# Kernel optimization log

Hardware: AMD Instinct MI355X
Metric: run time of the kernel (lower is better)

The kernel has to match this reference:

```python
import jax, jax.numpy as jnp
import numpy as np

N = 50000
E = 800000
T = 16
F_NODE = 8
VOCAB = 30000
D_TXT = 64
H = 64
C = 2


def _gru_last(emb, w_ih, w_hh, b_ih, b_hh):
    # emb: [N, T, D_TXT] -> last hidden state [N, H] (PyTorch GRU equations)
    def step(h, xt):
        gi = xt @ w_ih.T + b_ih          # [N, 3H]
        gh = h @ w_hh.T + b_hh           # [N, 3H]
        i_r, i_z, i_n = jnp.split(gi, 3, axis=-1)
        h_r, h_z, h_n = jnp.split(gh, 3, axis=-1)
        r = jax.nn.sigmoid(i_r + h_r)
        z = jax.nn.sigmoid(i_z + h_z)
        n = jnp.tanh(i_n + r * h_n)
        h_new = (1.0 - z) * n + z * h
        return h_new, None
    h0 = jnp.zeros((emb.shape[0], H), dtype=emb.dtype)
    hT, _ = jax.lax.scan(step, h0, jnp.swapaxes(emb, 0, 1))
    return hT


def _gcn_norm(edge_index, n_nodes):
    # add self-loops, symmetric normalization (PyG GCNConv default)
    loops = jnp.arange(n_nodes, dtype=edge_index.dtype)
    row = jnp.concatenate([edge_index[0], loops])
    col = jnp.concatenate([edge_index[1], loops])
    deg = jax.ops.segment_sum(jnp.ones_like(col, dtype=jnp.float32), col,
                              num_segments=n_nodes)
    dinv = jax.lax.rsqrt(jnp.maximum(deg, 1.0))
    norm = dinv[row] * dinv[col]
    return row, col, norm


def _gcn_conv(x, row, col, norm, W, b, n_nodes):
    m = x @ W                                    # [N, H]
    msg = norm[:, None] * m[row]                 # gather + scale
    out = jax.ops.segment_sum(msg, col, num_segments=n_nodes)
    return out + b


def setup_inputs() -> dict:
    key = jax.random.key(0)
    ks = jax.random.split(key, 16)
    s = 0.05
    return {
        "x": jax.random.normal(ks[0], (N, F_NODE), dtype=jnp.float32),
        "edge_index": jax.random.randint(ks[1], (2, E), 0, N, dtype=jnp.int32),
        "xtext": jax.random.randint(ks[2], (N, T), 0, VOCAB, dtype=jnp.int32),
        "embed": jax.random.normal(ks[3], (VOCAB, D_TXT), dtype=jnp.float32),
        "w_ih": jax.random.normal(ks[4], (3 * H, D_TXT), dtype=jnp.float32) * s,
        "w_hh": jax.random.normal(ks[5], (3 * H, H), dtype=jnp.float32) * s,
        "b_ih": jnp.zeros((3 * H,), dtype=jnp.float32),
        "b_hh": jnp.zeros((3 * H,), dtype=jnp.float32),
        "W1": jax.random.normal(ks[6], (F_NODE + H, H), dtype=jnp.float32) * s,
        "b1": jnp.zeros((H,), dtype=jnp.float32),
        "W2": jax.random.normal(ks[7], (H, H), dtype=jnp.float32) * s,
        "b2": jnp.zeros((H,), dtype=jnp.float32),
        "Wl1": jax.random.normal(ks[8], (2 * H, H), dtype=jnp.float32) * s,
        "bl1": jnp.zeros((H,), dtype=jnp.float32),
        "Wf": jax.random.normal(ks[9], (H, C), dtype=jnp.float32) * s,
        "bf": jnp.zeros((C,), dtype=jnp.float32),
    }


def reference(x, edge_index, xtext, embed, w_ih, w_hh, b_ih, b_hh,
              W1, b1, W2, b2, Wl1, bl1, Wf, bf):
    n_nodes = x.shape[0]
    # text encode: embedding lookup + GRU, take last timestep
    emb = embed[xtext]                               # [N, T, D_TXT]
    textout = _gru_last(emb, w_ih, w_hh, b_ih, b_hh)  # [N, H]
    h = jnp.concatenate([x, textout], axis=1)        # [N, F_NODE+H]
    # two GCN layers with shared normalized edge structure
    row, col, norm = _gcn_norm(edge_index, n_nodes)
    h = jax.nn.relu(_gcn_conv(h, row, col, norm, W1, b1, n_nodes))
    h = jax.nn.relu(_gcn_conv(h, row, col, norm, W2, b2, n_nodes))
    # edge-pair classifier (original edges, no self-loops)
    xpair = jnp.concatenate([h[edge_index[0]], h[edge_index[1]]], axis=1)
    xpair = jax.nn.relu(xpair @ Wl1 + bl1)
    logits = xpair @ Wf + bf
    return jax.nn.log_softmax(logits, axis=1)
```

## Files before the change

kernel.cpp:

```cpp
#include <hip/hip_runtime.h>
#include <math.h>

#define N_NODES 50000
#define N_EDGES 800000
#define SCAN_NB ((N_NODES + 255) / 256)
#define VOCAB   30000
#define NT32    ((N_NODES + 31) / 32)

typedef __attribute__((ext_vector_type(8)))  short bf16x8;
typedef __attribute__((ext_vector_type(4)))  float f32x4;
typedef __attribute__((ext_vector_type(16))) float f32x16;

__device__ inline short f2bf(float f) {
    union { float f; unsigned u; } v; v.f = f;
    unsigned r = v.u + 0x7FFFu + ((v.u >> 16) & 1u);
    return (short)(r >> 16);
}
__device__ inline float bflo(unsigned u) { union { unsigned u; float f; } v; v.u = u << 16; return v.f; }
__device__ inline float bfhi(unsigned u) { union { unsigned u; float f; } v; v.u = u & 0xffff0000u; return v.f; }
__device__ inline unsigned cvtpk(float a, float b) {
    unsigned r; asm("v_cvt_pk_bf16_f32 %0, %1, %2" : "=v"(r) : "v"(a), "v"(b)); return r;
}
__device__ inline float exp2neg(float x) { float r; asm("v_exp_f32 %0, -%1" : "=v"(r) : "v"(x)); return r; }
__device__ inline float exp2p(float x)   { float r; asm("v_exp_f32 %0, %1"  : "=v"(r) : "v"(x)); return r; }

__device__ inline f32x4 mfma16(bf16x8 a, bf16x8 b, f32x4 c) {
    return __builtin_amdgcn_mfma_f32_16x16x32_bf16(a, b, c, 0, 0, 0);
}
__device__ inline f32x16 mfma32(bf16x8 a, bf16x8 b, f32x16 c) {
    return __builtin_amdgcn_mfma_f32_32x32x16_bf16(a, b, c, 0, 0, 0);
}
__device__ inline f32x16 splat16(float v) {
    f32x16 r;
    #pragma unroll
    for (int i = 0; i < 16; ++i) r[i] = v;
    return r;
}

__global__ void k_embcvt(const float* __restrict__ e, short* __restrict__ o) {
    int i = blockIdx.x * 256 + threadIdx.x;
    if (i >= VOCAB * 64 / 8) return;
    const float4* p = (const float4*)(e + i * 8);
    float4 a = p[0], b = p[1];
    bf16x8 v;
    v[0]=f2bf(a.x); v[1]=f2bf(a.y); v[2]=f2bf(a.z); v[3]=f2bf(a.w);
    v[4]=f2bf(b.x); v[5]=f2bf(b.y); v[6]=f2bf(b.z); v[7]=f2bf(b.w);
    *(bf16x8*)(o + i * 8) = v;
}

__global__ void k_count(const int* __restrict__ ei, int* __restrict__ cnt) {
    int e = blockIdx.x * 256 + threadIdx.x;
    if (e < N_EDGES) atomicAdd(&cnt[ei[N_EDGES + e]], 1);
}
__global__ void k_scan_local(const int* __restrict__ cnt, int* __restrict__ excl,
                             int* __restrict__ bsum) {
    __shared__ int s[256];
    int tid = threadIdx.x;
    int i = blockIdx.x * 256 + tid;
    int v = (i < N_NODES) ? cnt[i] : 0;
    s[tid] = v;
    __syncthreads();
    #pragma unroll
    for (int off = 1; off < 256; off <<= 1) {
        int t = (tid >= off) ? s[tid - off] : 0;
        __syncthreads();
        s[tid] += t;
        __syncthreads();
    }
    if (i < N_NODES) excl[i] = s[tid] - v;
    if (tid == 255) bsum[blockIdx.x] = s[255];
}
__global__ void k_scan_bsum(int* __restrict__ bsum) {
    __shared__ int s[256];
    int tid = threadIdx.x;
    int v = (tid < SCAN_NB) ? bsum[tid] : 0;
    s[tid] = v;
    __syncthreads();
    #pragma unroll
    for (int off = 1; off < 256; off <<= 1) {
        int t = (tid >= off) ? s[tid - off] : 0;
        __syncthreads();
        s[tid] += t;
        __syncthreads();
    }
    if (tid < SCAN_NB) bsum[tid] = s[tid] - v;
}
__global__ void k_make_starts(const int* __restrict__ excl, const int* __restrict__ bsum,
                              const int* __restrict__ cnt,
                              int* __restrict__ starts, int* __restrict__ cursor,
                              float* __restrict__ dinv) {
    int i = blockIdx.x * 256 + threadIdx.x;
    if (i >= N_NODES) return;
    int st = excl[i] + bsum[blockIdx.x];
    starts[i] = st;
    cursor[i] = st;
    dinv[i] = rsqrtf((float)cnt[i] + 1.0f);
}
__global__ void k_fill(const int* __restrict__ ei, int* __restrict__ cursor,
                       int* __restrict__ csr_src) {
    int e = blockIdx.x * 256 + threadIdx.x;
    if (e >= N_EDGES) return;
    int c = ei[N_EDGES + e];
    int p = atomicAdd(&cursor[c], 1);
    csr_src[p] = ei[e];
}

__global__ __launch_bounds__(256) void k_gru8(
    const int*   __restrict__ xtext,
    const short* __restrict__ embbf,
    const float* __restrict__ w_ih, const float* __restrict__ w_hh,
    const float* __restrict__ b_ih, const float* __restrict__ b_hh,
    unsigned* __restrict__ ht32)
{
    __shared__ short bfrag[2 * 4 * 6 * 64 * 8];
    __shared__ short hbuf[4][32 * 64];

    const int tid = threadIdx.x;
    const float L2E = 1.4426950408889634f;
    for (int u = tid; u < 3072; u += 256) {
        int l   = u & 63;
        int ct  = (u >> 6) % 6;
        int ks  = (u / 384) % 4;
        int mat = u / 1536;
        const float* W = mat ? w_hh : w_ih;
        float sc = (ct < 4) ? L2E : 2.0f * L2E;
        const float* src = &W[(ct * 32 + (l & 31)) * 64 + ks * 16 + ((l >> 5) << 3)];
        short* dst = &bfrag[u * 8];
        #pragma unroll
        for (int i = 0; i < 8; ++i) dst[i] = f2bf(src[i] * sc);
    }
    __syncthreads();

    const int lane = tid & 63;
    const int wave = tid >> 6;
    const int l5 = lane >> 5;
    const int cl = lane & 31;

    const int tile  = blockIdx.x * 4 + wave;
    if (tile >= NT32) return;
    const int nbase = tile * 32;

    float b_r[2], b_z[2], b_ni[2], b_nh[2];
    #pragma unroll
    for (int p = 0; p < 2; ++p) {
        int j = p * 32 + cl;
        b_r[p]  = (b_ih[j]        + b_hh[j])        * L2E;
        b_z[p]  = (b_ih[64 + j]   + b_hh[64 + j])   * L2E;
        b_ni[p] = b_ih[128 + j] * (2.0f * L2E);
        b_nh[p] = b_hh[128 + j] * (2.0f * L2E);
    }

    const bf16x8* BF = (const bf16x8*)bfrag;
    short* hl = &hbuf[wave][0];

    float hr0[16], hr1[16];
    #pragma unroll
    for (int g = 0; g < 16; ++g) { hr0[g] = 0.0f; hr1[g] = 0.0f; }

    const int node = min(nbase + cl, N_NODES - 1);
    const int* toks = &xtext[node * 16];

    bf16x8 eA[4], eB[4];

#define LOADE(DST, T) { int tok_ = toks[T]; const short* er_ = &embbf[tok_ * 64 + 8 * l5]; \
    DST[0] = *(const bf16x8*)(er_);      DST[1] = *(const bf16x8*)(er_ + 16); \
    DST[2] = *(const bf16x8*)(er_ + 32); DST[3] = *(const bf16x8*)(er_ + 48); }

#define STEP(T, EC, EP, FIRST, LAST) { \
    bf16x8 hA[4]; \
    if (!(FIRST)) { \
        _Pragma("unroll") \
        for (int ks = 0; ks < 4; ++ks) { \
            int o = (ks * 2 + l5) ^ (cl & 7); \
            hA[ks] = *(const bf16x8*)&hl[cl * 64 + o * 8]; \
        } \
    } \
    if (!(LAST)) LOADE(EP, (T) + 1); \
    _Pragma("unroll") \
    for (int p = 0; p < 2; ++p) { \
        f32x16 ar = splat16(b_r[p]); \
        f32x16 az = splat16(b_z[p]); \
        f32x16 ai = splat16(b_ni[p]); \
        f32x16 ah = splat16(b_nh[p]); \
        _Pragma("unroll") \
        for (int ks = 0; ks < 4; ++ks) { \
            ar = mfma32(EC[ks], BF[(ks * 6 + p) * 64 + lane], ar); \
            az = mfma32(EC[ks], BF[(ks * 6 + 2 + p) * 64 + lane], az); \
            ai = mfma32(EC[ks], BF[(ks * 6 + 4 + p) * 64 + lane], ai); \
        } \
        if (!(FIRST)) { \
            _Pragma("unroll") \
            for (int ks = 0; ks < 4; ++ks) { \
                ar = mfma32(hA[ks], BF[((4 + ks) * 6 + p) * 64 + lane], ar); \
                az = mfma32(hA[ks], BF[((4 + ks) * 6 + 2 + p) * 64 + lane], az); \
                ah = mfma32(hA[ks], BF[((4 + ks) * 6 + 4 + p) * 64 + lane], ah); \
            } \
        } \
        float* hrp = p ? hr1 : hr0; \
        _Pragma("unroll") \
        for (int g = 0; g < 16; ++g) { \
            float r = __builtin_amdgcn_rcpf(1.0f + exp2neg(ar[g])); \
            float z = __builtin_amdgcn_rcpf(1.0f + exp2neg(az[g])); \
            float v = ai[g] + r * ah[g]; \
            float n = 1.0f - 2.0f * __builtin_amdgcn_rcpf(exp2p(v) + 1.0f); \
            hrp[g] = n + z * (hrp[g] - n); \
        } \
    } \
    _Pragma("unroll") \
    for (int g = 0; g < 16; ++g) { \
        unsigned u = cvtpk(hr0[g], hr1[g]); \
        int m = (g & 3) + 8 * (g >> 2) + 4 * l5; \
        if (!(LAST)) { \
            int o0 = (cl >> 3) ^ (m & 7); \
            int o1 = (4 + (cl >> 3)) ^ (m & 7); \
            hl[m * 64 + o0 * 8 + (cl & 7)] = (short)u; \
            hl[m * 64 + o1 * 8 + (cl & 7)] = (short)(u >> 16); \
        } else { \
            int n_ = nbase + m; \
            if (n_ < N_NODES) ht32[(unsigned)n_ * 32 + cl] = u; \
        } \
    } \
}

    LOADE(eA, 0);
    STEP(0, eA, eB, true, false)

    #pragma unroll 1
    for (int tt = 0; tt < 7; ++tt) {
        int t1 = 1 + 2 * tt;
        STEP(t1,     eB, eA, false, false)
        STEP(t1 + 1, eA, eB, false, false)
    }
    STEP(15, eB, eA, false, true)

#undef STEP
#undef LOADE
}

__global__ void k_mm1(const float* __restrict__ x, const unsigned* __restrict__ ht32,
                      const float* __restrict__ W, const float* __restrict__ dinv,
                      float* __restrict__ M) {
    __shared__ float Wl[72 * 64];
    int tid = threadIdx.x;
    for (int i = tid; i < 72 * 64; i += 256) Wl[i] = W[i];
    __syncthreads();
    int j = tid & 63;
    int n = blockIdx.x * 4 + (tid >> 6);
    if (n >= N_NODES) return;
    float acc = 0.0f;
    const float* xr = x + n * 8;
    #pragma unroll
    for (int k = 0; k < 8; ++k) acc += xr[k] * Wl[k * 64 + j];
    const unsigned* hr = ht32 + (unsigned)n * 32;
    #pragma unroll
    for (int w = 0; w < 32; ++w) {
        unsigned u = hr[w];
        acc += bflo(u) * Wl[(8 + w) * 64 + j];
        acc += bfhi(u) * Wl[(8 + 32 + w) * 64 + j];
    }
    M[n * 64 + j] = dinv[n] * acc;
}

__global__ void k_mm64(const float* __restrict__ X, const float* __restrict__ W,
                       const float* __restrict__ dinv, float* __restrict__ M) {
    __shared__ float Wl[64 * 64];
    int tid = threadIdx.x;
    for (int i = tid; i < 64 * 64; i += 256) Wl[i] = W[i];
    __syncthreads();
    int j = tid & 63;
    int n = blockIdx.x * 4 + (tid >> 6);
    if (n >= N_NODES) return;
    const float* xr = X + n * 64;
    float acc = 0.0f;
    #pragma unroll
    for (int k = 0; k < 64; ++k) acc += xr[k] * Wl[k * 64 + j];
    M[n * 64 + j] = dinv[n] * acc;
}

__global__ __launch_bounds__(256) void k_gather(
    const float* __restrict__ ms, const int* __restrict__ csr_src,
    const int* __restrict__ starts, const int* __restrict__ cnt,
    const float* __restrict__ dinv, const float* __restrict__ b,
    float* __restrict__ out)
{
    int n = blockIdx.x * 4 + (threadIdx.x >> 6);
    if (n >= N_NODES) return;
    int j = threadIdx.x & 63;
    int c = cnt[n];
    const int* lst = csr_src + starts[n];
    float acc = ms[n * 64 + j];
    int k = 0;
    for (; k + 8 <= c; k += 8) {
        int r[8];
        #pragma unroll
        for (int u = 0; u < 8; ++u) r[u] = lst[k + u];
        #pragma unroll
        for (int u = 0; u < 8; ++u) acc += ms[r[u] * 64 + j];
    }
    for (; k < c; ++k) acc += ms[lst[k] * 64 + j];
    float v = dinv[n] * acc + b[j];
    out[n * 64 + j] = fmaxf(v, 0.0f);
}

__global__ __launch_bounds__(256) void k_gather_bf(
    const float* __restrict__ ms, const int* __restrict__ csr_src,
    const int* __restrict__ starts, const int* __restrict__ cnt,
    const float* __restrict__ dinv, const float* __restrict__ b,
    short* __restrict__ out)
{
    int n = blockIdx.x * 4 + (threadIdx.x >> 6);
    if (n >= N_NODES) return;
    int j = threadIdx.x & 63;
    int c = cnt[n];
    const int* lst = csr_src + starts[n];
    float acc = ms[n * 64 + j];
    int k = 0;
    for (; k + 8 <= c; k += 8) {
        int r[8];
        #pragma unroll
        for (int u = 0; u < 8; ++u) r[u] = lst[k + u];
        #pragma unroll
        for (int u = 0; u < 8; ++u) acc += ms[r[u] * 64 + j];
    }
    for (; k < c; ++k) acc += ms[lst[k] * 64 + j];
    float v = dinv[n] * acc + b[j];
    out[n * 64 + j] = f2bf(fmaxf(v, 0.0f));
}

__global__ __launch_bounds__(256) void k_edge_mfma(
    const int* __restrict__ ei, const short* __restrict__ h2b,
    const float* __restrict__ Wl1, const float* __restrict__ bl1,
    const float* __restrict__ Wf,  const float* __restrict__ bf,
    float* __restrict__ out)
{
    __shared__ float wl_s[128 * 64];
    const int tid = threadIdx.x;
    for (int i = tid; i < 128 * 64; i += 256) wl_s[i] = Wl1[i];
    __syncthreads();

    const int lane = tid & 63;
    const int wave = tid >> 6;
    const int lg = lane >> 4;
    const int ll = lane & 15;

    bf16x8 B[16];
    #pragma unroll
    for (int ks = 0; ks < 4; ++ks) {
        #pragma unroll
        for (int ct = 0; ct < 4; ++ct) {
            int c  = ct * 16 + ll;
            int kb = ks * 32 + 8 * lg;
            bf16x8 v;
            #pragma unroll
            for (int i = 0; i < 8; ++i) v[i] = f2bf(wl_s[(kb + i) * 64 + c]);
            B[ks * 4 + ct] = v;
        }
    }
    float wf0[4], wf1[4], bl[4];
    #pragma unroll
    for (int ct = 0; ct < 4; ++ct) {
        int c = ct * 16 + ll;
        wf0[ct] = Wf[c * 2 + 0];
        wf1[ct] = Wf[c * 2 + 1];
        bl[ct]  = bl1[c];
    }
    const float bf0 = bf[0], bf1 = bf[1];

    for (int tile = blockIdx.x * 4 + wave; tile < N_EDGES / 16; tile += gridDim.x * 4) {
        const int ebase = tile * 16;
        const int erow  = ebase + ll;
        const int src = ei[erow];
        const int dst = ei[N_EDGES + erow];

        f32x4 acc[4];
        #pragma unroll
        for (int ct = 0; ct < 4; ++ct) acc[ct] = (f32x4){bl[ct], bl[ct], bl[ct], bl[ct]};

        #pragma unroll
        for (int ks = 0; ks < 4; ++ks) {
            const int nd = (ks < 2) ? src : dst;
            bf16x8 A = *(const bf16x8*)&h2b[nd * 64 + (ks & 1) * 32 + 8 * lg];
            #pragma unroll
            for (int ct = 0; ct < 4; ++ct) acc[ct] = mfma16(A, B[ks * 4 + ct], acc[ct]);
        }

        float p0[4], p1[4];
        #pragma unroll
        for (int q = 0; q < 4; ++q) { p0[q] = 0.0f; p1[q] = 0.0f; }
        #pragma unroll
        for (int ct = 0; ct < 4; ++ct) {
            #pragma unroll
            for (int q = 0; q < 4; ++q) {
                float hd = fmaxf(acc[ct][q], 0.0f);
                p0[q] += hd * wf0[ct];
                p1[q] += hd * wf1[ct];
            }
        }
        #pragma unroll
        for (int m = 1; m <= 8; m <<= 1) {
            #pragma unroll
            for (int q = 0; q < 4; ++q) {
                p0[q] += __shfl_xor(p0[q], m, 64);
                p1[q] += __shfl_xor(p1[q], m, 64);
            }
        }
        if (ll < 8) {
            int q = ll >> 1, cls = ll & 1;
            float l0 = p0[q] + bf0, l1 = p1[q] + bf1;
            float mx  = fmaxf(l0, l1);
            float lse = mx + __logf(__expf(l0 - mx) + __expf(l1 - mx));
            float val = (cls ? l1 : l0) - lse;
            out[(ebase + 4 * lg + q) * 2 + cls] = val;
        }
    }
}

extern "C" void kernel_launch(void* const* d_in, const int* in_sizes, int n_in,
                              void* d_out, int out_size, void* d_ws, size_t ws_size,
                              hipStream_t stream) {
    const float* x     = (const float*)d_in[0];
    const int*   ei    = (const int*)  d_in[1];
    const int*   xtext = (const int*)  d_in[2];
    const float* embed = (const float*)d_in[3];
    const float* w_ih  = (const float*)d_in[4];
    const float* w_hh  = (const float*)d_in[5];
    const float* b_ih  = (const float*)d_in[6];
    const float* b_hh  = (const float*)d_in[7];
    const float* W1    = (const float*)d_in[8];
    const float* b1    = (const float*)d_in[9];
    const float* W2    = (const float*)d_in[10];
    const float* b2    = (const float*)d_in[11];
    const float* Wl1   = (const float*)d_in[12];
    const float* bl1   = (const float*)d_in[13];
    const float* Wf    = (const float*)d_in[14];
    const float* bf    = (const float*)d_in[15];
    float* out = (float*)d_out;

    char* ws = (char*)d_ws;
    size_t off = 0;
    auto alloc = [&](size_t bytes) { char* p = ws + off; off += (bytes + 255) & ~size_t(255); return p; };
    unsigned* ht32   = (unsigned*)alloc(N_NODES * 32 * 4);
    float*    ms     = (float*)   alloc(N_NODES * 64 * 4);
    float*    h1     = (float*)   alloc(N_NODES * 64 * 4);
    short*    h2b    = (short*)   alloc(N_NODES * 64 * 2);
    float*    dinv   = (float*)   alloc(N_NODES * 4);
    int*      cnt    = (int*)     alloc(N_NODES * 4);
    int*      excl   = (int*)     alloc(N_NODES * 4);
    int*      starts = (int*)     alloc(N_NODES * 4);
    int*      cursor = (int*)     alloc(N_NODES * 4);
    int*      bsum   = (int*)     alloc(SCAN_NB * 4);
    int*      csr_src= (int*)     alloc(N_EDGES * 4);
    short*    embbf  = (short*)   alloc(VOCAB * 64 * 2);

    k_embcvt<<<(VOCAB * 64 / 8 + 255) / 256, 256, 0, stream>>>(embed, embbf);

    hipMemsetAsync(cnt, 0, N_NODES * 4, stream);
    k_count<<<(N_EDGES + 255) / 256, 256, 0, stream>>>(ei, cnt);
    k_scan_local<<<SCAN_NB, 256, 0, stream>>>(cnt, excl, bsum);
    k_scan_bsum<<<1, 256, 0, stream>>>(bsum);
    k_make_starts<<<SCAN_NB, 256, 0, stream>>>(excl, bsum, cnt, starts, cursor, dinv);
    k_fill<<<(N_EDGES + 255) / 256, 256, 0, stream>>>(ei, cursor, csr_src);

    k_gru8<<<(NT32 + 3) / 4, 256, 0, stream>>>(xtext, embbf, w_ih, w_hh, b_ih, b_hh, ht32);

    k_mm1<<<(N_NODES + 3) / 4, 256, 0, stream>>>(x, ht32, W1, dinv, ms);
    k_gather<<<(N_NODES + 3) / 4, 256, 0, stream>>>(ms, csr_src, starts, cnt, dinv, b1, h1);

    k_mm64<<<(N_NODES + 3) / 4, 256, 0, stream>>>(h1, W2, dinv, ms);
    k_gather_bf<<<(N_NODES + 3) / 4, 256, 0, stream>>>(ms, csr_src, starts, cnt, dinv, b2, h2b);

    k_edge_mfma<<<2048, 256, 0, stream>>>(ei, h2b, Wl1, bl1, Wf, bf, out);
}
```

Measured before the change: 381.8 us.

## Store GCN messages and hidden layer as packed bf16 pairs

The per-node messages and the first hidden layer are now stored as bf16 pairs, with feature j packed alongside feature j+32 in one 32-bit word, instead of fp32. This halves the bytes moved by the random-access neighbor gathers and by the dense matmul reads. Each gather now uses 32 lanes per node and 8 nodes per block. Rounding to bf16 before aggregation adds precision loss in both GCN layers.

New measurement: 353.4 us. -7.4%, faster.

```diff
diff --git a/kernel.cpp b/kernel.cpp
--- a/kernel.cpp
+++ b/kernel.cpp
@@ -239,7 +239,7 @@
 
 __global__ void k_mm1(const float* __restrict__ x, const unsigned* __restrict__ ht32,
                       const float* __restrict__ W, const float* __restrict__ dinv,
-                      float* __restrict__ M) {
+                      unsigned* __restrict__ msb) {
     __shared__ float Wl[72 * 64];
     int tid = threadIdx.x;
     for (int i = tid; i < 72 * 64; i += 256) Wl[i] = W[i];
@@ -258,11 +258,13 @@
         acc += bflo(u) * Wl[(8 + w) * 64 + j];
         acc += bfhi(u) * Wl[(8 + 32 + w) * 64 + j];
     }
-    M[n * 64 + j] = dinv[n] * acc;
-}
-
-__global__ void k_mm64(const float* __restrict__ X, const float* __restrict__ W,
-                       const float* __restrict__ dinv, float* __restrict__ M) {
+    acc *= dinv[n];
+    float part = __shfl_xor(acc, 32, 64);
+    if (j < 32) msb[(unsigned)n * 32 + j] = cvtpk(acc, part);
+}
+
+__global__ void k_mm64b(const unsigned* __restrict__ Xp, const float* __restrict__ W,
+                        const float* __restrict__ dinv, unsigned* __restrict__ msb) {
     __shared__ float Wl[64 * 64];
     int tid = threadIdx.x;
     for (int i = tid; i < 64 * 64; i += 256) Wl[i] = W[i];
@@ -270,61 +272,85 @@
     int j = tid & 63;
     int n = blockIdx.x * 4 + (tid >> 6);
     if (n >= N_NODES) return;
-    const float* xr = X + n * 64;
+    const unsigned* xr = Xp + (unsigned)n * 32;
     float acc = 0.0f;
     #pragma unroll
-    for (int k = 0; k < 64; ++k) acc += xr[k] * Wl[k * 64 + j];
-    M[n * 64 + j] = dinv[n] * acc;
-}
-
-__global__ __launch_bounds__(256) void k_gather(
-    const float* __restrict__ ms, const int* __restrict__ csr_src,
+    for (int w = 0; w < 32; ++w) {
+        unsigned u = xr[w];
+        acc += bflo(u) * Wl[w * 64 + j];
+        acc += bfhi(u) * Wl[(w + 32) * 64 + j];
+    }
+    acc *= dinv[n];
+    float part = __shfl_xor(acc, 32, 64);
+    if (j < 32) msb[(unsigned)n * 32 + j] = cvtpk(acc, part);
+}
+
+__global__ __launch_bounds__(256) void k_gather_p(
+    const unsigned* __restrict__ msb, const int* __restrict__ csr_src,
     const int* __restrict__ starts, const int* __restrict__ cnt,
     const float* __restrict__ dinv, const float* __restrict__ b,
-    float* __restrict__ out)
+    unsigned* __restrict__ outp)
 {
-    int n = blockIdx.x * 4 + (threadIdx.x >> 6);
+    int n = blockIdx.x * 8 + (threadIdx.x >> 5);
     if (n >= N_NODES) return;
-    int j = threadIdx.x & 63;
+    int w = threadIdx.x & 31;
     int c = cnt[n];
     const int* lst = csr_src + starts[n];
-    float acc = ms[n * 64 + j];
+    unsigned us = msb[(unsigned)n * 32 + w];
+    float a0 = bflo(us), a1 = bfhi(us);
     int k = 0;
-    for (; k + 8 <= c; k += 8) {
-        int r[8];
-        #pragma unroll
-        for (int u = 0; u < 8; ++u) r[u] = lst[k + u];
-        #pragma unroll
-        for (int u = 0; u < 8; ++u) acc += ms[r[u] * 64 + j];
-    }
-    for (; k < c; ++k) acc += ms[lst[k] * 64 + j];
-    float v = dinv[n] * acc + b[j];
-    out[n * 64 + j] = fmaxf(v, 0.0f);
-}
-
-__global__ __launch_bounds__(256) void k_gather_bf(
-    const float* __restrict__ ms, const int* __restrict__ csr_src,
+    for (; k + 4 <= c; k += 4) {
+        int r0 = lst[k], r1 = lst[k+1], r2 = lst[k+2], r3 = lst[k+3];
+        unsigned u0 = msb[(unsigned)r0 * 32 + w];
+        unsigned u1 = msb[(unsigned)r1 * 32 + w];
+        unsigned u2 = msb[(unsigned)r2 * 32 + w];
+        unsigned u3 = msb[(unsigned)r3 * 32 + w];
+        a0 += bflo(u0) + bflo(u1) + bflo(u2) + bflo(u3);
+        a1 += bfhi(u0) + bfhi(u1) + bfhi(u2) + bfhi(u3);
+    }
+    for (; k < c; ++k) {
+        unsigned u = msb[(unsigned)lst[k] * 32 + w];
+        a0 += bflo(u); a1 += bfhi(u);
+    }
+    float d = dinv[n];
+    float v0 = fmaxf(d * a0 + b[w], 0.0f);
+    float v1 = fmaxf(d * a1 + b[w + 32], 0.0f);
+    outp[(unsigned)n * 32 + w] = cvtpk(v0, v1);
+}
+
+__global__ __launch_bounds__(256) void k_gather_h2(
+    const unsigned* __restrict__ msb, const int* __restrict__ csr_src,
     const int* __restrict__ starts, const int* __restrict__ cnt,
     const float* __restrict__ dinv, const float* __restrict__ b,
     short* __restrict__ out)
 {
-    int n = blockIdx.x * 4 + (threadIdx.x >> 6);
+    int n = blockIdx.x * 8 + (threadIdx.x >> 5);
     if (n >= N_NODES) return;
-    int j = threadIdx.x & 63;
+    int w = threadIdx.x & 31;
     int c = cnt[n];
     const int* lst = csr_src + starts[n];
-    float acc = ms[n * 64 + j];
+    unsigned us = msb[(unsigned)n * 32 + w];
+    float a0 = bflo(us), a1 = bfhi(us);
     int k = 0;
-    for (; k + 8 <= c; k += 8) {
-        int r[8];
-        #pragma unroll
-        for (int u = 0; u < 8; ++u) r[u] = lst[k + u];
-        #pragma unroll
-        for (int u = 0; u < 8; ++u) acc += ms[r[u] * 64 + j];
-    }
-    for (; k < c; ++k) acc += ms[lst[k] * 64 + j];
-    float v = dinv[n] * acc + b[j];
-    out[n * 64 + j] = f2bf(fmaxf(v, 0.0f));
+    for (; k + 4 <= c; k += 4) {
+        int r0 = lst[k], r1 = lst[k+1], r2 = lst[k+2], r3 = lst[k+3];
+        unsigned u0 = msb[(unsigned)r0 * 32 + w];
+        unsigned u1 = msb[(unsigned)r1 * 32 + w];
+        unsigned u2 = msb[(unsigned)r2 * 32 + w];
+        unsigned u3 = msb[(unsigned)r3 * 32 + w];
+        a0 += bflo(u0) + bflo(u1) + bflo(u2) + bflo(u3);
+        a1 += bfhi(u0) + bfhi(u1) + bfhi(u2) + bfhi(u3);
+    }
+    for (; k < c; ++k) {
+        unsigned u = msb[(unsigned)lst[k] * 32 + w];
+        a0 += bflo(u); a1 += bfhi(u);
+    }
+    float d = dinv[n];
+    float v0 = fmaxf(d * a0 + b[w], 0.0f);
+    float v1 = fmaxf(d * a1 + b[w + 32], 0.0f);
+    unsigned u = cvtpk(v0, v1);
+    out[(unsigned)n * 64 + w]      = (short)u;
+    out[(unsigned)n * 64 + 32 + w] = (short)(u >> 16);
 }
 
 __global__ __launch_bounds__(256) void k_edge_mfma(
@@ -440,8 +466,8 @@
     size_t off = 0;
     auto alloc = [&](size_t bytes) { char* p = ws + off; off += (bytes + 255) & ~size_t(255); return p; };
     unsigned* ht32   = (unsigned*)alloc(N_NODES * 32 * 4);
-    float*    ms     = (float*)   alloc(N_NODES * 64 * 4);
-    float*    h1     = (float*)   alloc(N_NODES * 64 * 4);
+    unsigned* msb    = (unsigned*)alloc(N_NODES * 32 * 4);
+    unsigned* h1b    = (unsigned*)alloc(N_NODES * 32 * 4);
     short*    h2b    = (short*)   alloc(N_NODES * 64 * 2);
     float*    dinv   = (float*)   alloc(N_NODES * 4);
     int*      cnt    = (int*)     alloc(N_NODES * 4);
@@ -463,11 +489,11 @@
 
     k_gru8<<<(NT32 + 3) / 4, 256, 0, stream>>>(xtext, embbf, w_ih, w_hh, b_ih, b_hh, ht32);
 
-    k_mm1<<<(N_NODES + 3) / 4, 256, 0, stream>>>(x, ht32, W1, dinv, ms);
-    k_gather<<<(N_NODES + 3) / 4, 256, 0, stream>>>(ms, csr_src, starts, cnt, dinv, b1, h1);
-
-    k_mm64<<<(N_NODES + 3) / 4, 256, 0, stream>>>(h1, W2, dinv, ms);
-    k_gather_bf<<<(N_NODES + 3) / 4, 256, 0, stream>>>(ms, csr_src, starts, cnt, dinv, b2, h2b);
+    k_mm1<<<(N_NODES + 3) / 4, 256, 0, stream>>>(x, ht32, W1, dinv, msb);
+    k_gather_p<<<(N_NODES + 7) / 8, 256, 0, stream>>>(msb, csr_src, starts, cnt, dinv, b1, h1b);
+
+    k_mm64b<<<(N_NODES + 3) / 4, 256, 0, stream>>>(h1b, W2, dinv, msb);
+    k_gather_h2<<<(N_NODES + 7) / 8, 256, 0, stream>>>(msb, csr_src, starts, cnt, dinv, b2, h2b);
 
     k_edge_mfma<<<2048, 256, 0, stream>>>(ei, h2b, Wl1, bl1, Wf, bf, out);
 }
```
